# Kernel optimization log

Measured on AMD Instinct MI355X. Metric: run time of the kernel, lower is better.

The kernel has to match this reference:

```python
import jax, jax.numpy as jnp
import numpy as np
from jax import lax

IN_REP = 32   # in_repres_dim (hardcoded in module)
OUT_REP = 8   # out_repres_dim (hardcoded in module)


def conv2d(x, w, b, stride, pad):
    # x: (N,C,H,W), w: (O,I,kh,kw)
    y = lax.conv_general_dilated(x, w, (stride, stride), [(pad, pad), (pad, pad)],
                                 dimension_numbers=('NCHW', 'OIHW', 'NCHW'))
    return y + b[None, :, None, None]


def hopfield_retrieve(tokens, memory, Wv, Wo):
    # Modern-Hopfield lookup layer, single head, static stored & state patterns:
    # Q = tokens, K = memory (learned lookup patterns), V = memory @ Wv,
    # beta = 1/sqrt(d), single update step, output projection Wo.
    d = memory.shape[-1]
    scores = jnp.einsum('bnd,md->bnm', tokens, memory) / jnp.sqrt(jnp.asarray(d, tokens.dtype))
    assoc = jax.nn.softmax(scores, axis=-1)          # (B, N, M) retrieval weights
    V = memory @ Wv                                   # (M, d)
    return jnp.einsum('bnm,md->bnd', assoc, V) @ Wo   # (B, N, d)


def setup_inputs() -> dict:
    key = jax.random.key(0)
    ks = jax.random.split(key, 6)
    B, Cin, Cout, Q = 4, 3, 64, 512
    x = jax.random.normal(ks[0], (B, Cin, IN_REP, IN_REP), jnp.float32)
    conv1_w = jax.random.normal(ks[1], (Cout // 2, Cin, 4, 4), jnp.float32) * 0.1
    conv1_b = jnp.zeros((Cout // 2,), jnp.float32)
    conv2_w = jax.random.normal(ks[2], (Cout, Cout // 2, 4, 4), jnp.float32) * 0.05
    conv2_b = jnp.zeros((Cout,), jnp.float32)
    lookup = jax.random.normal(ks[3], (Q, Cout), jnp.float32) * 0.1
    Wv = jax.random.normal(ks[4], (Cout, Cout), jnp.float32) * 0.1
    Wo = jax.random.normal(ks[5], (Cout, Cout), jnp.float32) * 0.1
    return {"x": x, "conv1_w": conv1_w, "conv1_b": conv1_b,
            "conv2_w": conv2_w, "conv2_b": conv2_b,
            "lookup": lookup, "Wv": Wv, "Wo": Wo}


def reference(x, conv1_w, conv1_b, conv2_w, conv2_b, lookup, Wv, Wo):
    B, Cin = x.shape[0], x.shape[1]
    Cout = conv2_w.shape[0]

    def propagate(xi):  # (Cin, 32, 32) -> (Cout, 8, 8): the conv encoder path
        z1 = jax.nn.relu(conv2d(xi[None], conv1_w, conv1_b, 2, 1))
        z2 = jax.nn.relu(conv2d(z1, conv2_w, conv2_b, 2, 1))
        return z2[0]

    # Per-sample full jacobian of the encoder: (B, Cout, 8, 8, Cin, 32, 32)
    J = jax.vmap(jax.jacrev(propagate))(x)
    J = J.reshape(B, Cout, OUT_REP * OUT_REP, Cin, IN_REP * IN_REP)
    # permute(0,3,4,1,2) -> (B, Cin, 1024, Cout, 64)
    Jm = jnp.transpose(J, (0, 3, 4, 1, 2))

    xf = x.reshape(B, Cin, IN_REP * IN_REP)
    # contract input against its own encoder jacobian -> (B, Cout, 64)
    z_q_masked = jnp.einsum('abc,abcde->ade', xf, Jm)

    tokens = jnp.transpose(z_q_masked, (0, 2, 1))          # (B, 64, Cout)
    out = hopfield_retrieve(tokens, lookup, Wv, Wo)        # (B, 64, Cout)
    out = jnp.transpose(out, (0, 2, 1))
    return out.reshape(B, Cout, OUT_REP, OUT_REP)
```

## Files before the change

### kernel.cpp

```cpp
#include <hip/hip_runtime.h>


__global__ __launch_bounds__(256) void k1_conv1_and_V(
    const float* __restrict__ x, const float* __restrict__ w1,
    const float* __restrict__ b1, const float* __restrict__ lookup,
    const float* __restrict__ Wv,
    float* __restrict__ z1, float* __restrict__ t1m, float* __restrict__ V) {
  int blk = blockIdx.x, tid = threadIdx.x;
  if (blk < 128) {
    __shared__ float xs[3072];
    int b = blk >> 5, c1 = blk & 31;
    const float4* xsrc = (const float4*)(x + b * 3072);
    float4* xdst = (float4*)xs;
#pragma unroll
    for (int i = 0; i < 3; ++i) xdst[tid + i * 256] = xsrc[tid + i * 256];
    __syncthreads();
    int oh = tid >> 4, ow = tid & 15;
    int iw0 = ow * 2 - 1;
    float acc = 0.f;
#pragma unroll
    for (int ci = 0; ci < 3; ++ci) {
      const float* xp = xs + ci * 1024;
      const float4* wp = (const float4*)(w1 + (c1 * 3 + ci) * 16);
      float4 wr0 = wp[0], wr1 = wp[1], wr2 = wp[2], wr3 = wp[3];
#pragma unroll
      for (int kh = 0; kh < 4; ++kh) {
        int ih = oh * 2 - 1 + kh;
        if ((unsigned)ih < 32u) {
          float4 wk = (kh == 0) ? wr0 : (kh == 1) ? wr1 : (kh == 2) ? wr2 : wr3;
          const float* row = xp + ih * 32;
          if (iw0 >= 0)      acc += row[iw0]     * wk.x;
                             acc += row[iw0 + 1] * wk.y;
                             acc += row[iw0 + 2] * wk.z;
          if (iw0 + 3 < 32)  acc += row[iw0 + 3] * wk.w;
        }
      }
    }
    float pre = acc + b1[c1];
    bool on = pre > 0.f;
    int o = ((b * 32 + c1) << 8) + tid;
    z1[o]  = on ? pre : 0.f;
    t1m[o] = on ? acc : 0.f;
  } else {
    int u = ((blk - 128) << 8) + tid;
    int m = u >> 6, d = u & 63;
    const float* lp = lookup + m * 64;
    float acc = 0.f;
#pragma unroll
    for (int k = 0; k < 64; ++k) acc += lp[k] * Wv[k * 64 + d];
    V[u] = acc;
  }
}

__global__ __launch_bounds__(256) void k2_conv2_tokens(
    const float* __restrict__ z1, const float* __restrict__ t1m,
    const float* __restrict__ w2, const float* __restrict__ b2,
    float* __restrict__ tokens) {
  __shared__ float2 ZT[8192];
  int tid = threadIdx.x;
  int b = blockIdx.x >> 6, c2 = blockIdx.x & 63;

  const float4* z4 = (const float4*)(z1 + (b << 13));
  const float4* t4 = (const float4*)(t1m + (b << 13));
#pragma unroll
  for (int i = 0; i < 8; ++i) {
    int f = tid + (i << 8);
    float4 zv = z4[f], tv = t4[f];
    int c1 = f >> 6;
    int i0 = (f & 63) << 2;
    int s = c1 & 15;
    int perm = s & 3;
    float2 e0 = {zv.x, tv.x}, e1 = {zv.y, tv.y}, e2 = {zv.z, tv.z}, e3 = {zv.w, tv.w};
    if (perm & 1) { float2 t = e0; e0 = e1; e1 = t; t = e2; e2 = e3; e3 = t; }
    if (perm & 2) { float2 t = e0; e0 = e2; e2 = t; t = e1; e1 = e3; e3 = t; }
    float2* dst = &ZT[(c1 << 8) + (i0 ^ (s & 12))];
    dst[0] = e0; dst[1] = e1; dst[2] = e2; dst[3] = e3;
  }
  __syncthreads();

  int g = tid & 3, p = tid >> 2;
  int oh = p >> 3, ow = p & 7;
  int iw0 = ow * 2 - 1;
  float accz = 0.f, acct = 0.f;
#pragma unroll
  for (int j = 0; j < 8; ++j) {
    int c1 = g + (j << 2);
    int s = c1 & 15;
    const float2* zp = &ZT[c1 << 8];
    const float4* wp = (const float4*)(w2 + ((c2 * 32 + c1) << 4));
    float4 wr0 = wp[0], wr1 = wp[1], wr2 = wp[2], wr3 = wp[3];
#pragma unroll
    for (int kh = 0; kh < 4; ++kh) {
      int ih = oh * 2 - 1 + kh;
      if ((unsigned)ih < 16u) {
        float4 wk = (kh == 0) ? wr0 : (kh == 1) ? wr1 : (kh == 2) ? wr2 : wr3;
        int base = ih << 4;
        if (iw0 >= 0) { float2 v = zp[(base + iw0) ^ s];     accz += v.x * wk.x; acct += v.y * wk.x; }
        {               float2 v = zp[(base + iw0 + 1) ^ s]; accz += v.x * wk.y; acct += v.y * wk.y; }
        {               float2 v = zp[(base + iw0 + 2) ^ s]; accz += v.x * wk.z; acct += v.y * wk.z; }
        if (iw0 + 3 < 16) { float2 v = zp[(base + iw0 + 3) ^ s]; accz += v.x * wk.w; acct += v.y * wk.w; }
      }
    }
  }
  accz += __shfl_xor(accz, 1); acct += __shfl_xor(acct, 1);
  accz += __shfl_xor(accz, 2); acct += __shfl_xor(acct, 2);
  if (g == 0) {
    float pre = accz + b2[c2];
    tokens[(b << 12) + (c2 << 6) + p] = (pre > 0.f) ? acct : 0.f;
  }
}

__global__ __launch_bounds__(256) void k3_hopfield(
    const float* __restrict__ tokens, const float* __restrict__ lookup,
    const float* __restrict__ V, const float* __restrict__ Wo,
    float* __restrict__ out) {
  __shared__ float tok[64];
  __shared__ float prob[512];
  __shared__ float redbuf[8];
  __shared__ float part[4][64];
  __shared__ float yv[64];
  int tid = threadIdx.x;
  int b = blockIdx.x >> 6, n = blockIdx.x & 63;

  if (tid < 64) tok[tid] = tokens[(b << 12) + (tid << 6) + n];
  __syncthreads();

  int q = tid >> 2, l = tid & 3, w = tid >> 6;
  const float4* tk4 = (const float4*)tok;
  float4 ta = tk4[(l << 2) + 0], tb = tk4[(l << 2) + 1],
         tc = tk4[(l << 2) + 2], td = tk4[(l << 2) + 3];
  float sc[8];
#pragma unroll
  for (int i = 0; i < 8; ++i) {
    int m = q + (i << 6);
    const float4* lp = (const float4*)(lookup + (m << 6)) + (l << 2);
    float4 A = lp[0], B = lp[1], C = lp[2], D = lp[3];
    float s = A.x * ta.x + A.y * ta.y + A.z * ta.z + A.w * ta.w
            + B.x * tb.x + B.y * tb.y + B.z * tb.z + B.w * tb.w
            + C.x * tc.x + C.y * tc.y + C.z * tc.z + C.w * tc.w
            + D.x * td.x + D.y * td.y + D.z * td.z + D.w * td.w;
    s += __shfl_xor(s, 1);
    s += __shfl_xor(s, 2);
    sc[i] = s * 0.125f;
  }
  float mx = sc[0];
#pragma unroll
  for (int i = 1; i < 8; ++i) mx = fmaxf(mx, sc[i]);
  mx = fmaxf(mx, __shfl_xor(mx, 4));
  mx = fmaxf(mx, __shfl_xor(mx, 8));
  mx = fmaxf(mx, __shfl_xor(mx, 16));
  mx = fmaxf(mx, __shfl_xor(mx, 32));
  if ((tid & 63) == 0) redbuf[w] = mx;
  __syncthreads();
  mx = fmaxf(fmaxf(redbuf[0], redbuf[1]), fmaxf(redbuf[2], redbuf[3]));

  float e[8];
  float sum = 0.f;
#pragma unroll
  for (int i = 0; i < 8; ++i) { e[i] = __expf(sc[i] - mx); sum += e[i]; }
  if (l != 0) sum = 0.f;
  sum += __shfl_xor(sum, 1);
  sum += __shfl_xor(sum, 2);
  sum += __shfl_xor(sum, 4);
  sum += __shfl_xor(sum, 8);
  sum += __shfl_xor(sum, 16);
  sum += __shfl_xor(sum, 32);
  if ((tid & 63) == 0) redbuf[4 + w] = sum;
  if (l == 0) {
#pragma unroll
    for (int i = 0; i < 8; ++i) prob[q + (i << 6)] = e[i];
  }
  __syncthreads();
  float inv = 1.f / (redbuf[4] + redbuf[5] + redbuf[6] + redbuf[7]);

  int d = tid & 63;
  float acc = 0.f;
  const float* vp = V + (w << 7) * 64 + d;
#pragma unroll 4
  for (int m = 0; m < 128; ++m) acc += prob[(w << 7) + m] * vp[m << 6];
  part[w][d] = acc;
  __syncthreads();
  if (tid < 64)
    yv[tid] = (part[0][tid] + part[1][tid] + part[2][tid] + part[3][tid]) * inv;
  __syncthreads();

  float po = 0.f;
#pragma unroll
  for (int k = 0; k < 16; ++k) {
    int d2 = (w << 4) + k;
    po += yv[d2] * Wo[(d2 << 6) + d];
  }
  __syncthreads();
  part[w][d] = po;
  __syncthreads();
  if (tid < 64)
    out[(b << 12) + (tid << 6) + n] =
        part[0][tid] + part[1][tid] + part[2][tid] + part[3][tid];
}

extern "C" void kernel_launch(void* const* d_in, const int* in_sizes, int n_in,
                              void* d_out, int out_size, void* d_ws, size_t ws_size,
                              hipStream_t stream) {
  const float* x      = (const float*)d_in[0];
  const float* w1     = (const float*)d_in[1];
  const float* b1     = (const float*)d_in[2];
  const float* w2     = (const float*)d_in[3];
  const float* b2     = (const float*)d_in[4];
  const float* lookup = (const float*)d_in[5];
  const float* Wv     = (const float*)d_in[6];
  const float* Wo     = (const float*)d_in[7];

  float* ws     = (float*)d_ws;
  float* z1     = ws;
  float* t1m    = ws + 32768;
  float* V      = ws + 65536;
  float* tokens = ws + 98304;
  float* out    = (float*)d_out;

  k1_conv1_and_V<<<256, 256, 0, stream>>>(x, w1, b1, lookup, Wv, z1, t1m, V);
  k2_conv2_tokens<<<256, 256, 0, stream>>>(z1, t1m, w2, b2, tokens);
  k3_hopfield<<<256, 256, 0, stream>>>(tokens, lookup, V, Wo, out);
}
```

Baseline: 95.01 us.

## Fuse conv encoder and Hopfield retrieval into one per-token kernel

Replaces the three launches with a single kernel where each block handles one output token (batch, spatial position). The block recomputes only the 4x4 receptive-field patch of conv1 it needs, runs conv2 for all 64 channels at that position, and then does the Hopfield softmax retrieval. The precomputed V = lookup@Wv matrix is replaced by reassociation: the block computes prob@lookup first and then multiplies by Wv. This removes two launches and the global-memory round trips for z1, t1m, V and tokens, at the cost of redundant conv1 work and redundant staging of x and w1 in every block.

Result: faster. 82.07 us (-13.6%).

```diff
diff --git a/kernel.cpp b/kernel.cpp
--- a/kernel.cpp
+++ b/kernel.cpp
@@ -1,134 +1,102 @@
 #include <hip/hip_runtime.h>
 
 
-__global__ __launch_bounds__(256) void k1_conv1_and_V(
+__global__ __launch_bounds__(256) void fused_all(
     const float* __restrict__ x, const float* __restrict__ w1,
-    const float* __restrict__ b1, const float* __restrict__ lookup,
-    const float* __restrict__ Wv,
-    float* __restrict__ z1, float* __restrict__ t1m, float* __restrict__ V) {
-  int blk = blockIdx.x, tid = threadIdx.x;
-  if (blk < 128) {
-    __shared__ float xs[3072];
-    int b = blk >> 5, c1 = blk & 31;
+    const float* __restrict__ b1, const float* __restrict__ w2,
+    const float* __restrict__ b2, const float* __restrict__ lookup,
+    const float* __restrict__ Wv, const float* __restrict__ Wo,
+    float* __restrict__ out) {
+  __shared__ float xs[3072];
+  __shared__ float ws1[32 * 49];
+  __shared__ float2 zt[512];
+  __shared__ float4 tok4[16];
+  __shared__ float prob[512];
+  __shared__ float redbuf[8];
+  __shared__ float part[4][64];
+  __shared__ float vec[64];
+
+  int tid = threadIdx.x;
+  int b = blockIdx.x >> 6, n = blockIdx.x & 63;
+  int Oh = n >> 3, Ow = n & 7;
+
+  {
     const float4* xsrc = (const float4*)(x + b * 3072);
     float4* xdst = (float4*)xs;
 #pragma unroll
     for (int i = 0; i < 3; ++i) xdst[tid + i * 256] = xsrc[tid + i * 256];
-    __syncthreads();
-    int oh = tid >> 4, ow = tid & 15;
-    int iw0 = ow * 2 - 1;
-    float acc = 0.f;
 #pragma unroll
-    for (int ci = 0; ci < 3; ++ci) {
-      const float* xp = xs + ci * 1024;
-      const float4* wp = (const float4*)(w1 + (c1 * 3 + ci) * 16);
-      float4 wr0 = wp[0], wr1 = wp[1], wr2 = wp[2], wr3 = wp[3];
-#pragma unroll
-      for (int kh = 0; kh < 4; ++kh) {
-        int ih = oh * 2 - 1 + kh;
-        if ((unsigned)ih < 32u) {
-          float4 wk = (kh == 0) ? wr0 : (kh == 1) ? wr1 : (kh == 2) ? wr2 : wr3;
-          const float* row = xp + ih * 32;
-          if (iw0 >= 0)      acc += row[iw0]     * wk.x;
-                             acc += row[iw0 + 1] * wk.y;
-                             acc += row[iw0 + 2] * wk.z;
-          if (iw0 + 3 < 32)  acc += row[iw0 + 3] * wk.w;
-        }
-      }
+    for (int i = 0; i < 6; ++i) {
+      int idx = tid + (i << 8);
+      int c1 = idx / 48, r = idx - c1 * 48;
+      ws1[c1 * 49 + r] = w1[idx];
     }
-    float pre = acc + b1[c1];
-    bool on = pre > 0.f;
-    int o = ((b * 32 + c1) << 8) + tid;
-    z1[o]  = on ? pre : 0.f;
-    t1m[o] = on ? acc : 0.f;
-  } else {
-    int u = ((blk - 128) << 8) + tid;
-    int m = u >> 6, d = u & 63;
-    const float* lp = lookup + m * 64;
-    float acc = 0.f;
-#pragma unroll
-    for (int k = 0; k < 64; ++k) acc += lp[k] * Wv[k * 64 + d];
-    V[u] = acc;
-  }
-}
-
-__global__ __launch_bounds__(256) void k2_conv2_tokens(
-    const float* __restrict__ z1, const float* __restrict__ t1m,
-    const float* __restrict__ w2, const float* __restrict__ b2,
-    float* __restrict__ tokens) {
-  __shared__ float2 ZT[8192];
-  int tid = threadIdx.x;
-  int b = blockIdx.x >> 6, c2 = blockIdx.x & 63;
-
-  const float4* z4 = (const float4*)(z1 + (b << 13));
-  const float4* t4 = (const float4*)(t1m + (b << 13));
-#pragma unroll
-  for (int i = 0; i < 8; ++i) {
-    int f = tid + (i << 8);
-    float4 zv = z4[f], tv = t4[f];
-    int c1 = f >> 6;
-    int i0 = (f & 63) << 2;
-    int s = c1 & 15;
-    int perm = s & 3;
-    float2 e0 = {zv.x, tv.x}, e1 = {zv.y, tv.y}, e2 = {zv.z, tv.z}, e3 = {zv.w, tv.w};
-    if (perm & 1) { float2 t = e0; e0 = e1; e1 = t; t = e2; e2 = e3; e3 = t; }
-    if (perm & 2) { float2 t = e0; e0 = e2; e2 = t; t = e1; e1 = e3; e3 = t; }
-    float2* dst = &ZT[(c1 << 8) + (i0 ^ (s & 12))];
-    dst[0] = e0; dst[1] = e1; dst[2] = e2; dst[3] = e3;
   }
   __syncthreads();
 
-  int g = tid & 3, p = tid >> 2;
-  int oh = p >> 3, ow = p & 7;
-  int iw0 = ow * 2 - 1;
-  float accz = 0.f, acct = 0.f;
 #pragma unroll
-  for (int j = 0; j < 8; ++j) {
-    int c1 = g + (j << 2);
-    int s = c1 & 15;
-    const float2* zp = &ZT[c1 << 8];
-    const float4* wp = (const float4*)(w2 + ((c2 * 32 + c1) << 4));
-    float4 wr0 = wp[0], wr1 = wp[1], wr2 = wp[2], wr3 = wp[3];
+  for (int i = 0; i < 2; ++i) {
+    int u = tid + (i << 8);
+    int c1 = u & 31, k = u >> 5;
+    int kh = k >> 2, kw = k & 3;
+    int mh = 2 * Oh - 1 + kh, mw = 2 * Ow - 1 + kw;
+    float z = 0.f, t = 0.f;
+    if (((unsigned)mh < 16u) && ((unsigned)mw < 16u)) {
+      float acc = 0.f;
+      int ih0 = 2 * mh - 1, iw0 = 2 * mw - 1;
 #pragma unroll
-    for (int kh = 0; kh < 4; ++kh) {
-      int ih = oh * 2 - 1 + kh;
-      if ((unsigned)ih < 16u) {
-        float4 wk = (kh == 0) ? wr0 : (kh == 1) ? wr1 : (kh == 2) ? wr2 : wr3;
-        int base = ih << 4;
-        if (iw0 >= 0) { float2 v = zp[(base + iw0) ^ s];     accz += v.x * wk.x; acct += v.y * wk.x; }
-        {               float2 v = zp[(base + iw0 + 1) ^ s]; accz += v.x * wk.y; acct += v.y * wk.y; }
-        {               float2 v = zp[(base + iw0 + 2) ^ s]; accz += v.x * wk.z; acct += v.y * wk.z; }
-        if (iw0 + 3 < 16) { float2 v = zp[(base + iw0 + 3) ^ s]; accz += v.x * wk.w; acct += v.y * wk.w; }
+      for (int ci = 0; ci < 3; ++ci) {
+        const float* xp = xs + ci * 1024;
+        const float* wp = ws1 + c1 * 49 + ci * 16;
+#pragma unroll
+        for (int r = 0; r < 4; ++r) {
+          int ih = ih0 + r;
+          if ((unsigned)ih < 32u) {
+            const float* row = xp + ih * 32;
+            if (iw0 >= 0)     acc += row[iw0]     * wp[r * 4 + 0];
+                              acc += row[iw0 + 1] * wp[r * 4 + 1];
+                              acc += row[iw0 + 2] * wp[r * 4 + 2];
+            if (iw0 + 3 < 32) acc += row[iw0 + 3] * wp[r * 4 + 3];
+          }
+        }
+      }
+      float pre = acc + b1[c1];
+      if (pre > 0.f) { z = pre; t = acc; }
+    }
+    zt[k * 32 + c1] = make_float2(z, t);
+  }
+  __syncthreads();
+
+  {
+    int c2 = tid >> 2, g = tid & 3;
+    float accz = 0.f, acct = 0.f;
+#pragma unroll
+    for (int j = 0; j < 8; ++j) {
+      int c1 = g + (j << 2);
+      const float4* wp = (const float4*)(w2 + ((c2 * 32 + c1) << 4));
+      float wk[16];
+      *(float4*)(wk + 0) = wp[0]; *(float4*)(wk + 4) = wp[1];
+      *(float4*)(wk + 8) = wp[2]; *(float4*)(wk + 12) = wp[3];
+      const float2* zp = zt + c1;
+#pragma unroll
+      for (int k = 0; k < 16; ++k) {
+        float2 v = zp[k << 5];
+        accz += v.x * wk[k];
+        acct += v.y * wk[k];
       }
     }
+    accz += __shfl_xor(accz, 1); acct += __shfl_xor(acct, 1);
+    accz += __shfl_xor(accz, 2); acct += __shfl_xor(acct, 2);
+    if (g == 0) {
+      float pre = accz + b2[c2];
+      ((float*)tok4)[c2] = (pre > 0.f) ? acct : 0.f;
+    }
   }
-  accz += __shfl_xor(accz, 1); acct += __shfl_xor(acct, 1);
-  accz += __shfl_xor(accz, 2); acct += __shfl_xor(acct, 2);
-  if (g == 0) {
-    float pre = accz + b2[c2];
-    tokens[(b << 12) + (c2 << 6) + p] = (pre > 0.f) ? acct : 0.f;
-  }
-}
-
-__global__ __launch_bounds__(256) void k3_hopfield(
-    const float* __restrict__ tokens, const float* __restrict__ lookup,
-    const float* __restrict__ V, const float* __restrict__ Wo,
-    float* __restrict__ out) {
-  __shared__ float tok[64];
-  __shared__ float prob[512];
-  __shared__ float redbuf[8];
-  __shared__ float part[4][64];
-  __shared__ float yv[64];
-  int tid = threadIdx.x;
-  int b = blockIdx.x >> 6, n = blockIdx.x & 63;
-
-  if (tid < 64) tok[tid] = tokens[(b << 12) + (tid << 6) + n];
   __syncthreads();
 
   int q = tid >> 2, l = tid & 3, w = tid >> 6;
-  const float4* tk4 = (const float4*)tok;
-  float4 ta = tk4[(l << 2) + 0], tb = tk4[(l << 2) + 1],
-         tc = tk4[(l << 2) + 2], td = tk4[(l << 2) + 3];
+  float4 ta = tok4[(l << 2) + 0], tb = tok4[(l << 2) + 1],
+         tc = tok4[(l << 2) + 2], td = tok4[(l << 2) + 3];
   float sc[8];
 #pragma unroll
   for (int i = 0; i < 8; ++i) {
@@ -175,20 +143,33 @@
 
   int d = tid & 63;
   float acc = 0.f;
-  const float* vp = V + (w << 7) * 64 + d;
+  const float* lp = lookup + ((w << 7) << 6) + d;
 #pragma unroll 4
-  for (int m = 0; m < 128; ++m) acc += prob[(w << 7) + m] * vp[m << 6];
+  for (int m = 0; m < 128; ++m) acc += prob[(w << 7) + m] * lp[m << 6];
   part[w][d] = acc;
   __syncthreads();
   if (tid < 64)
-    yv[tid] = (part[0][tid] + part[1][tid] + part[2][tid] + part[3][tid]) * inv;
+    vec[tid] = (part[0][tid] + part[1][tid] + part[2][tid] + part[3][tid]) * inv;
   __syncthreads();
 
   float po = 0.f;
 #pragma unroll
   for (int k = 0; k < 16; ++k) {
     int d2 = (w << 4) + k;
-    po += yv[d2] * Wo[(d2 << 6) + d];
+    po += vec[d2] * Wv[(d2 << 6) + d];
+  }
+  __syncthreads();
+  part[w][d] = po;
+  __syncthreads();
+  if (tid < 64)
+    vec[tid] = part[0][tid] + part[1][tid] + part[2][tid] + part[3][tid];
+  __syncthreads();
+
+  po = 0.f;
+#pragma unroll
+  for (int k = 0; k < 16; ++k) {
+    int d2 = (w << 4) + k;
+    po += vec[d2] * Wo[(d2 << 6) + d];
   }
   __syncthreads();
   part[w][d] = po;
@@ -209,15 +190,7 @@
   const float* lookup = (const float*)d_in[5];
   const float* Wv     = (const float*)d_in[6];
   const float* Wo     = (const float*)d_in[7];
+  float* out = (float*)d_out;
 
-  float* ws     = (float*)d_ws;
-  float* z1     = ws;
-  float* t1m    = ws + 32768;
-  float* V      = ws + 65536;
-  float* tokens = ws + 98304;
-  float* out    = (float*)d_out;
-
-  k1_conv1_and_V<<<256, 256, 0, stream>>>(x, w1, b1, lookup, Wv, z1, t1m, V);
-  k2_conv2_tokens<<<256, 256, 0, stream>>>(z1, t1m, w2, b2, tokens);
-  k3_hopfield<<<256, 256, 0, stream>>>(tokens, lookup, V, Wo, out);
+  fused_all<<<256, 256, 0, stream>>>(x, w1, b1, w2, b2, lookup, Wv, Wo, out);
 }
```
